# Performance work log

Hardware: AMD Instinct MI355X
Metric: run time of the kernel (lower is better)

Reference implementation:

```python
import jax, jax.numpy as jnp
import numpy as np

B, S, D, H = 2, 2048, 2048, 16
Dh = D // H


def _rotate_interleaved(t):
    # t: (..., Dh); pairs (x0,x1) -> (-x1, x0), interleaved
    t2 = t.reshape(t.shape[:-1] + (Dh // 2, 2))
    rot = jnp.stack([-t2[..., 1], t2[..., 0]], axis=-1)
    return rot.reshape(t.shape)


def _apply_rope(t, cos, sin):
    # t: (B,H,S,Dh); cos/sin: (S,Dh) broadcast over batch and heads
    return t * cos[None, None, :, :] + _rotate_interleaved(t) * sin[None, None, :, :]


def setup_inputs() -> dict:
    key = jax.random.key(0)
    ks = jax.random.split(key, 4)
    x = jax.random.normal(ks[0], (B, S, D), dtype=jnp.float32)
    wq = jax.random.normal(ks[1], (D, D), dtype=jnp.float32) * (D ** -0.5)
    wk = jax.random.normal(ks[2], (D, D), dtype=jnp.float32) * (D ** -0.5)
    wv = jax.random.normal(ks[3], (D, D), dtype=jnp.float32) * (D ** -0.5)
    # Real RoPE cos/sin tables: theta_i = 10000^{-2i/Dh}, interleaved layout
    inv_freq = 1.0 / (10000.0 ** (np.arange(0, Dh, 2, dtype=np.float32) / Dh))
    angles = np.arange(S, dtype=np.float32)[:, None] * inv_freq[None, :]  # (S, Dh/2)
    angles = np.repeat(angles, 2, axis=-1)  # (S, Dh) interleaved
    rope_cos = jnp.asarray(np.cos(angles))
    rope_sin = jnp.asarray(np.sin(angles))
    return {"x": x, "wq": wq, "wk": wk, "wv": wv,
            "rope_cos": rope_cos, "rope_sin": rope_sin}


def reference(x, wq, wk, wv, rope_cos, rope_sin):
    b, s, d = x.shape
    # QKV projections (torch Linear: y = x @ W^T), split into heads -> (B,H,S,Dh)
    def proj(w):
        return (x @ w.T).reshape(b, s, H, Dh).transpose(0, 2, 1, 3)
    q, k, v = proj(wq), proj(wk), proj(wv)
    cos, sin = rope_cos[:s], rope_sin[:s]
    q = _apply_rope(q, cos, sin)
    k = _apply_rope(k, cos, sin)
    # causal SDPA
    scores = jnp.einsum('bhqd,bhkd->bhqk', q, k) / jnp.sqrt(jnp.float32(Dh))
    causal = jnp.tril(jnp.ones((s, s), dtype=bool))
    scores = jnp.where(causal[None, None], scores, jnp.float32(-1e30))
    attn = jax.nn.softmax(scores, axis=-1)
    out = jnp.einsum('bhqk,bhkd->bhqd', attn, v)  # (B,H,S,Dh)
    # extra trailing softmax over head dim (as in source)
    out = jax.nn.softmax(out.astype(jnp.float32), axis=-1)
    return out.transpose(0, 2, 1, 3).reshape(b, s, -1)
```

## Files before the change

kernel.cpp:

```cpp
#include <hip/hip_runtime.h>

#define Bc 2
#define Sc 2048
#define Dc 2048
#define Hc 16
#define DHc 128

typedef _Float16 f16;
typedef __attribute__((ext_vector_type(4))) _Float16 v4h;
typedef __attribute__((ext_vector_type(8))) _Float16 v8h;
typedef __attribute__((ext_vector_type(4))) float v4f;
typedef __attribute__((ext_vector_type(16))) float v16f;
typedef __attribute__((ext_vector_type(4))) float f32x4;

__global__ void cvt_kernel(const float* __restrict__ x, const float* __restrict__ wq,
                           const float* __restrict__ wk, const float* __restrict__ wv,
                           f16* __restrict__ xh, f16* __restrict__ wqh,
                           f16* __restrict__ wkh, f16* __restrict__ wvh)
{
    int bid = blockIdx.x;
    const float* src; f16* dst; int idx;
    if (bid < 8192)       { src = x;  dst = xh;  idx = bid; }
    else if (bid < 12288) { src = wq; dst = wqh; idx = bid - 8192; }
    else if (bid < 16384) { src = wk; dst = wkh; idx = bid - 12288; }
    else                  { src = wv; dst = wvh; idx = bid - 16384; }
    int i = idx * 256 + threadIdx.x;
    f32x4 v = ((const f32x4*)src)[i];
    v4h hv; hv[0]=(f16)v[0]; hv[1]=(f16)v[1]; hv[2]=(f16)v[2]; hv[3]=(f16)v[3];
    ((v4h*)dst)[i] = hv;
}

__launch_bounds__(512, 2)
__global__ void proj256_kernel(const f16* __restrict__ xh, const f16* __restrict__ wall,
                               const float* __restrict__ cs, const float* __restrict__ sn,
                               f16* __restrict__ qh, f16* __restrict__ kh,
                               f16* __restrict__ vt)
{
    const int bid = blockIdx.x;
    const int swz = (bid & 7) * 96 + (bid >> 3);
    const int mt = swz & 31, nt = swz >> 5;
    const int m0 = mt * 128, n0 = nt * 256;

    const int tid = threadIdx.x;
    const int wid = tid >> 6, lane = tid & 63;
    const int wr = wid >> 2, wc = wid & 3;
    const int l15 = lane & 15, quad = lane >> 4;
    const int x7 = l15 & 7;

    __shared__ __align__(16) f16 lds[73728];

    const f16* aS[2]; const f16* bS[4];
    #pragma unroll
    for (int j = 0; j < 2; ++j) {
        int c = tid + j * 512;
        int r = c >> 3, s = c & 7;
        aS[j] = xh + (size_t)(m0 + r) * Dc + ((s ^ (r & 7)) * 8);
    }
    #pragma unroll
    for (int j = 0; j < 4; ++j) {
        int c = tid + j * 512;
        int r = c >> 3, s = c & 7;
        bS[j] = wall + (size_t)(n0 + r) * Dc + ((s ^ (r & 7)) * 8);
    }

#define STAGE(kt_, buf_) do {                                                   \
        const int _ko = (kt_) * 64;                                             \
        f16* _b = lds + (buf_) * 24576;                                         \
        _Pragma("unroll")                                                       \
        for (int j = 0; j < 2; ++j)                                             \
            __builtin_amdgcn_global_load_lds(                                   \
                (const __attribute__((address_space(1))) void*)(aS[j] + _ko),   \
                (__attribute__((address_space(3))) void*)(_b + j * 4096 + wid * 512), \
                16, 0, 0);                                                      \
        _Pragma("unroll")                                                       \
        for (int j = 0; j < 4; ++j)                                             \
            __builtin_amdgcn_global_load_lds(                                   \
                (const __attribute__((address_space(1))) void*)(bS[j] + _ko),   \
                (__attribute__((address_space(3))) void*)(_b + 8192 + j * 4096 + wid * 512), \
                16, 0, 0);                                                      \
    } while (0)

#define VMW12 asm volatile("s_waitcnt vmcnt(12)" ::: "memory")
#define VMW6  asm volatile("s_waitcnt vmcnt(6)"  ::: "memory")
#define VMW0  asm volatile("s_waitcnt vmcnt(0)"  ::: "memory")
#define LGKM0 asm volatile("s_waitcnt lgkmcnt(0)" ::: "memory")
#define BAR   __builtin_amdgcn_s_barrier()

    v4f acc[4][4];
    #pragma unroll
    for (int i = 0; i < 4; ++i)
        #pragma unroll
        for (int j = 0; j < 4; ++j)
            acc[i][j] = (v4f){0.f, 0.f, 0.f, 0.f};

    STAGE(0, 0);
    STAGE(1, 1);

    int bR = 0;
    int bSt = 2;

    #pragma unroll 1
    for (int t = 0; t < 32; ++t) {
        if (t + 2 < 32) { STAGE(t + 2, bSt); VMW12; }
        else if (t + 1 < 32) { VMW6; }
        else { VMW0; }
        BAR;

        {
            const f16* _Ab = lds + bR * 24576;
            const f16* _Bb = _Ab + 8192;
            v8h af[2][4], bf[2][4];
            #pragma unroll
            for (int kk = 0; kk < 2; ++kk) {
                #pragma unroll
                for (int mi = 0; mi < 4; ++mi)
                    af[kk][mi] = *(const v8h*)(_Ab + (wr * 64 + mi * 16 + l15) * 64
                                               + (((kk * 4 + quad) ^ x7) * 8));
                #pragma unroll
                for (int ni = 0; ni < 4; ++ni)
                    bf[kk][ni] = *(const v8h*)(_Bb + (wc * 64 + ni * 16 + l15) * 64
                                               + (((kk * 4 + quad) ^ x7) * 8));
            }
            __builtin_amdgcn_s_setprio(1);
            #pragma unroll
            for (int kk = 0; kk < 2; ++kk)
                #pragma unroll
                for (int mi = 0; mi < 4; ++mi)
                    #pragma unroll
                    for (int ni = 0; ni < 4; ++ni)
                        acc[mi][ni] = __builtin_amdgcn_mfma_f32_16x16x32_f16(
                            af[kk][mi], bf[kk][ni], acc[mi][ni], 0, 0, 0);
            __builtin_amdgcn_s_setprio(0);
        }

        LGKM0;
        BAR;

        bR  = (bR  == 2) ? 0 : bR  + 1;
        bSt = (bSt == 2) ? 0 : bSt + 1;
    }

#undef STAGE
#undef VMW12
#undef VMW6
#undef VMW0
#undef LGKM0
#undef BAR

    const int z = n0 >> 11;
    const int bb = m0 >> 11, s0 = m0 & 2047;

    if (z < 2) {
        f16 (*Ep)[264] = (f16(*)[264])lds;
        #pragma unroll
        for (int mi = 0; mi < 4; ++mi)
            #pragma unroll
            for (int ni = 0; ni < 4; ++ni)
                #pragma unroll
                for (int r = 0; r < 4; ++r)
                    Ep[wr * 64 + mi * 16 + quad * 4 + r][wc * 64 + ni * 16 + l15] =
                        (f16)acc[mi][ni][r];
        __syncthreads();
        f16* outp = (z == 0) ? qh : kh;
        const float scl = (z == 0) ? 0.08838834764831845f : 1.0f;
        #pragma unroll
        for (int it = 0; it < 8; ++it) {
            int ch = tid + it * 512, row = ch >> 5, c = ch & 31;
            v8h val = *(const v8h*)&Ep[row][c * 8];
            int s = s0 + row;
            int nn = (n0 & 2047) + c * 8;
            int h = nn >> 7, d0 = nn & 127;
            const float* cp = cs + (size_t)s * DHc + d0;
            const float* sp = sn + (size_t)s * DHc + d0;
            f32x4 ca = *(const f32x4*)cp, cb = *(const f32x4*)(cp + 4);
            f32x4 sa = *(const f32x4*)sp, sb = *(const f32x4*)(sp + 4);
            float v[8];
            #pragma unroll
            for (int j = 0; j < 8; ++j) v[j] = (float)val[j];
            v8h rv;
            rv[0] = (f16)((v[0]*ca[0] - v[1]*sa[0]) * scl);
            rv[1] = (f16)((v[1]*ca[1] + v[0]*sa[1]) * scl);
            rv[2] = (f16)((v[2]*ca[2] - v[3]*sa[2]) * scl);
            rv[3] = (f16)((v[3]*ca[3] + v[2]*sa[3]) * scl);
            rv[4] = (f16)((v[4]*cb[0] - v[5]*sb[0]) * scl);
            rv[5] = (f16)((v[5]*cb[1] + v[4]*sb[1]) * scl);
            rv[6] = (f16)((v[6]*cb[2] - v[7]*sb[2]) * scl);
            rv[7] = (f16)((v[7]*cb[3] + v[6]*sb[3]) * scl);
            *(v8h*)(outp + ((size_t)(bb * Hc + h) * Sc + s) * DHc + d0) = rv;
        }
    } else {
        f16 (*Ep)[136] = (f16(*)[136])lds;
        #pragma unroll
        for (int mi = 0; mi < 4; ++mi)
            #pragma unroll
            for (int ni = 0; ni < 4; ++ni)
                #pragma unroll
                for (int r = 0; r < 4; ++r)
                    Ep[wc * 64 + ni * 16 + l15][wr * 64 + mi * 16 + quad * 4 + r] =
                        (f16)acc[mi][ni][r];
        __syncthreads();
        #pragma unroll
        for (int it = 0; it < 8; ++it) {
            int ch = tid + it * 512, n = ch >> 4, cm = ch & 15;
            int nn = (n0 & 2047) + n;
            int h = nn >> 7, d = nn & 127;
            int s = s0 + cm * 8;
            *(v8h*)(vt + ((size_t)(bb * Hc + h) * DHc + d) * Sc + s) =
                *(const v8h*)&Ep[n][cm * 8];
        }
    }
}

__launch_bounds__(256)
__global__ void proj_kernel(const float* __restrict__ x, const float* __restrict__ wq,
                            const float* __restrict__ wk, const float* __restrict__ wv,
                            f16* __restrict__ qh, f16* __restrict__ kh, f16* __restrict__ vt)
{
    const int z = blockIdx.z;
    const float* w = (z == 0) ? wq : ((z == 1) ? wk : wv);
    const int m0 = blockIdx.x * 128, n0 = blockIdx.y * 128;
    const int tid = threadIdx.x, lane = tid & 63, wid = tid >> 6;
    const int wm = wid >> 1, wn = wid & 1;
    const int l15 = lane & 15, quad = lane >> 4;

    __shared__ __align__(16) f16 smem[2 * 128 * 72];
    f16 (*As)[72] = (f16(*)[72])smem;
    f16 (*Bs)[72] = (f16(*)[72])(smem + 128 * 72);

    v4f acc[4][4];
    for (int i = 0; i < 4; ++i)
        for (int j = 0; j < 4; ++j)
            acc[i][j] = (v4f){0.f, 0.f, 0.f, 0.f};

    for (int k0 = 0; k0 < Dc; k0 += 64) {
        __syncthreads();
        for (int it = 0; it < 4; ++it) {
            int chunk = tid + it * 256;
            int r = chunk >> 3, cc = chunk & 7;
            const f32x4* pa = (const f32x4*)(x + (size_t)(m0 + r) * Dc + k0 + cc * 8);
            f32x4 a0 = pa[0], a1 = pa[1];
            v8h ha;
            ha[0]=(f16)a0[0]; ha[1]=(f16)a0[1]; ha[2]=(f16)a0[2]; ha[3]=(f16)a0[3];
            ha[4]=(f16)a1[0]; ha[5]=(f16)a1[1]; ha[6]=(f16)a1[2]; ha[7]=(f16)a1[3];
            *(v8h*)&As[r][cc * 8] = ha;
            const f32x4* pb = (const f32x4*)(w + (size_t)(n0 + r) * Dc + k0 + cc * 8);
            f32x4 b0 = pb[0], b1 = pb[1];
            v8h hb;
            hb[0]=(f16)b0[0]; hb[1]=(f16)b0[1]; hb[2]=(f16)b0[2]; hb[3]=(f16)b0[3];
            hb[4]=(f16)b1[0]; hb[5]=(f16)b1[1]; hb[6]=(f16)b1[2]; hb[7]=(f16)b1[3];
            *(v8h*)&Bs[r][cc * 8] = hb;
        }
        __syncthreads();
        for (int kk = 0; kk < 2; ++kk) {
            v8h af[4], bf[4];
            for (int mi = 0; mi < 4; ++mi)
                af[mi] = *(const v8h*)&As[wm * 64 + mi * 16 + l15][kk * 32 + quad * 8];
            for (int ni = 0; ni < 4; ++ni)
                bf[ni] = *(const v8h*)&Bs[wn * 64 + ni * 16 + l15][kk * 32 + quad * 8];
            for (int mi = 0; mi < 4; ++mi)
                for (int ni = 0; ni < 4; ++ni)
                    acc[mi][ni] = __builtin_amdgcn_mfma_f32_16x16x32_f16(
                        af[mi], bf[ni], acc[mi][ni], 0, 0, 0);
        }
    }
    __syncthreads();
    f16 (*Ep)[136] = (f16(*)[136])smem;
    for (int mi = 0; mi < 4; ++mi)
        for (int ni = 0; ni < 4; ++ni)
            for (int r = 0; r < 4; ++r) {
                int ml = wm * 64 + mi * 16 + quad * 4 + r;
                int nl = wn * 64 + ni * 16 + l15;
                f16 val = (f16)acc[mi][ni][r];
                if (z == 2) Ep[nl][ml] = val;
                else        Ep[ml][nl] = val;
            }
    __syncthreads();
    const int b = m0 >> 11, s0 = m0 & 2047, h = n0 >> 7;
    if (z < 2) {
        f16* outp = (z == 0) ? qh : kh;
        for (int it = 0; it < 8; ++it) {
            int ch = tid + it * 256, row = ch >> 4, c = ch & 15;
            *(v8h*)(outp + ((size_t)((b * Hc + h) * Sc) + s0 + row) * DHc + c * 8) =
                *(const v8h*)&Ep[row][c * 8];
        }
    } else {
        for (int it = 0; it < 8; ++it) {
            int ch = tid + it * 256, row = ch >> 4, c = ch & 15;
            *(v8h*)(vt + ((size_t)((b * Hc + h) * DHc) + row) * Sc + s0 + c * 8) =
                *(const v8h*)&Ep[row][c * 8];
        }
    }
}

__global__ void rope_kernel(f16* __restrict__ qh, f16* __restrict__ kh,
                            const float* __restrict__ cs, const float* __restrict__ sn)
{
    int i  = blockIdx.x * 256 + threadIdx.x;
    int d2 = i & 63;
    int s  = (i >> 6) & (Sc - 1);
    int bh = i >> 17;
    f16* t = blockIdx.y ? kh : qh;
    float scale = blockIdx.y ? 1.0f : 0.08838834764831845f;
    float c  = cs[s * DHc + 2 * d2];
    float sv = sn[s * DHc + 2 * d2];
    f16* p = t + ((size_t)bh * Sc + s) * DHc + 2 * d2;
    float t0 = (float)p[0], t1 = (float)p[1];
    p[0] = (f16)((t0 * c - t1 * sv) * scale);
    p[1] = (f16)((t1 * c + t0 * sv) * scale);
}

__launch_bounds__(256, 2)
__global__ void attn_kernel(const f16* __restrict__ qh, const f16* __restrict__ kh,
                            const f16* __restrict__ vt, float* __restrict__ out)
{
    const int L = blockIdx.x;
    const int slot = L >> 3;
    const int bh = (L & 7) * 4 + (slot >> 3);
    const int p  = slot & 7;
    const int b = bh >> 4, h = bh & 15;
    const int tid = threadIdx.x, lane = tid & 63, w = tid >> 6;
    const int l31 = lane & 31, half = lane >> 5;
    const int sw = l31 & 7;

    __shared__ __align__(16) f16 smem[32768];
    f16* ksm = smem;
    f16* vsm = smem + 16384;

    const size_t bhoff = (size_t)bh * Sc * DHc;

    const f16* ksrc[4]; const f16* vsrc[4];
    f16* kdst[4]; f16* vdst[4];
    #pragma unroll
    for (int j = 0; j < 4; ++j) {
        int slot0 = j * 256 + w * 64;
        {   int r = (slot0 >> 4) + (lane >> 4);
            int c = (lane & 15) ^ (r & 7);
            ksrc[j] = kh + bhoff + (size_t)r * DHc + c * 8;
            kdst[j] = ksm + slot0 * 8; }
        {   int r = (slot0 >> 3) + (lane >> 3);
            int c = (lane & 7) ^ (r & 7);
            vsrc[j] = vt + bhoff + (size_t)r * Sc + c * 8;
            vdst[j] = vsm + slot0 * 8; }
    }

#define STAGE(kt_, buf_) do {                                                   \
        int _ko = (kt_) * 64 * DHc;                                             \
        int _vo = (kt_) * 64;                                                   \
        int _lb = (buf_) * 8192;                                                \
        _Pragma("unroll")                                                       \
        for (int j = 0; j < 4; ++j) {                                           \
            __builtin_amdgcn_global_load_lds(                                   \
                (const __attribute__((address_space(1))) void*)(ksrc[j] + _ko), \
                (__attribute__((address_space(3))) void*)(kdst[j] + _lb), 16, 0, 0); \
            __builtin_amdgcn_global_load_lds(                                   \
                (const __attribute__((address_space(1))) void*)(vsrc[j] + _vo), \
                (__attribute__((address_space(3))) void*)(vdst[j] + _lb), 16, 0, 0); \
        } } while (0)

    const int qtA = 15 - p;
    const int nktA = 2 * qtA + 2;

    int ibuf = 0;
    STAGE(0, 0);

    #pragma unroll 1
    for (int ph = 0; ph < 2; ++ph) {
        const int qt  = ph ? p : qtA;
        const int nkt = 2 * qt + 2;
        const int q0  = qt * 128 + w * 32;
        const int qg  = q0 + l31;

        v8h qf[8];
        const f16* qrow = qh + bhoff + (size_t)qg * DHc;
        #pragma unroll
        for (int s = 0; s < 8; ++s)
            qf[s] = *(const v8h*)(qrow + s * 16 + half * 8);

        float l_run = 0.f;
        v16f o[4];
        #pragma unroll
        for (int i = 0; i < 4; ++i)
            #pragma unroll
            for (int r = 0; r < 16; ++r) o[i][r] = 0.f;

        #pragma unroll 1
        for (int kt = 0; kt < nkt; ++kt, ++ibuf) {
            __syncthreads();
            const int buf = ibuf & 1;
            const int ni = ibuf + 1;
            if (ni < 34) {
                int tn = (ni < nktA) ? ni : ni - nktA;
                STAGE(tn, ni & 1);
            }
            if (q0 + 31 < kt * 64) continue;

            const f16* kbuf = ksm + buf * 8192;
            const f16* vbuf = vsm + buf * 8192;
            const bool do1 = (kt * 64 + 32 <= q0 + 31);

            v16f st0, st1;
            #pragma unroll
            for (int r = 0; r < 16; ++r) { st0[r] = 0.f; st1[r] = 0.f; }
            #pragma unroll
            for (int s = 0; s < 8; ++s) {
                int c = ((s * 2 + half) ^ sw) * 8;
                v8h kf0 = *(const v8h*)(kbuf + l31 * 128 + c);
                st0 = __builtin_amdgcn_mfma_f32_32x32x16_f16(kf0, qf[s], st0, 0, 0, 0);
                if (do1) {
                    v8h kf1 = *(const v8h*)(kbuf + (32 + l31) * 128 + c);
                    st1 = __builtin_amdgcn_mfma_f32_32x32x16_f16(kf1, qf[s], st1, 0, 0, 0);
                }
            }

            float sum = 0.f;
            #pragma unroll
            for (int r = 0; r < 16; ++r) {
                int key = kt * 64 + (r & 3) + 8 * (r >> 2) + 4 * half;
                float sv = (key > qg) ? -1e30f : st0[r];
                float pe = __expf(sv);
                st0[r] = pe; sum += pe;
            }
            if (do1) {
                #pragma unroll
                for (int r = 0; r < 16; ++r) {
                    int key = kt * 64 + 32 + (r & 3) + 8 * (r >> 2) + 4 * half;
                    float sv = (key > qg) ? -1e30f : st1[r];
                    float pe = __expf(sv);
                    st1[r] = pe; sum += pe;
                }
            }
            sum += __shfl_xor(sum, 32);
            l_run += sum;

            #pragma unroll
            for (int s2 = 0; s2 < 4; ++s2) {
                v4h bfr;
                bfr[0]=(f16)st0[4*s2]; bfr[1]=(f16)st0[4*s2+1];
                bfr[2]=(f16)st0[4*s2+2]; bfr[3]=(f16)st0[4*s2+3];
                int c = ((s2 ^ sw) * 8) + half * 4;
                #pragma unroll
                for (int dt = 0; dt < 4; ++dt) {
                    v4h vf = *(const v4h*)(vbuf + (dt * 32 + l31) * 64 + c);
                    o[dt] = __builtin_amdgcn_mfma_f32_32x32x8f16(vf, bfr, o[dt], 0, 0, 0);
                }
            }
            if (do1) {
                #pragma unroll
                for (int s2 = 0; s2 < 4; ++s2) {
                    v4h bfr;
                    bfr[0]=(f16)st1[4*s2]; bfr[1]=(f16)st1[4*s2+1];
                    bfr[2]=(f16)st1[4*s2+2]; bfr[3]=(f16)st1[4*s2+3];
                    int c = (((4 + s2) ^ sw) * 8) + half * 4;
                    #pragma unroll
                    for (int dt = 0; dt < 4; ++dt) {
                        v4h vf = *(const v4h*)(vbuf + (dt * 32 + l31) * 64 + c);
                        o[dt] = __builtin_amdgcn_mfma_f32_32x32x8f16(vf, bfr, o[dt], 0, 0, 0);
                    }
                }
            }
        }

        float inv = 1.f / l_run;
        float mxd = -1e30f;
        #pragma unroll
        for (int dt = 0; dt < 4; ++dt)
            #pragma unroll
            for (int r = 0; r < 16; ++r) {
                o[dt][r] *= inv;
                mxd = fmaxf(mxd, o[dt][r]);
            }
        mxd = fmaxf(mxd, __shfl_xor(mxd, 32));
        float sd = 0.f;
        #pragma unroll
        for (int dt = 0; dt < 4; ++dt)
            #pragma unroll
            for (int r = 0; r < 16; ++r) {
                float t = __expf(o[dt][r] - mxd);
                o[dt][r] = t;
                sd += t;
            }
        sd += __shfl_xor(sd, 32);
        float rinv = 1.f / sd;

        float* orow = out + (size_t)(b * Sc + qg) * Dc + h * DHc;
        #pragma unroll
        for (int dt = 0; dt < 4; ++dt)
            #pragma unroll
            for (int g = 0; g < 4; ++g) {
                f32x4 vv;
                vv[0] = o[dt][4*g+0] * rinv;
                vv[1] = o[dt][4*g+1] * rinv;
                vv[2] = o[dt][4*g+2] * rinv;
                vv[3] = o[dt][4*g+3] * rinv;
                *(f32x4*)(orow + dt * 32 + g * 8 + half * 4) = vv;
            }
    }
#undef STAGE
}

extern "C" void kernel_launch(void* const* d_in, const int* in_sizes, int n_in,
                              void* d_out, int out_size, void* d_ws, size_t ws_size,
                              hipStream_t stream)
{
    const float* x  = (const float*)d_in[0];
    const float* wq = (const float*)d_in[1];
    const float* wk = (const float*)d_in[2];
    const float* wv = (const float*)d_in[3];
    const float* cs = (const float*)d_in[4];
    const float* sn = (const float*)d_in[5];
    float* out = (float*)d_out;

    const size_t tsz = (size_t)Bc * Hc * Sc * DHc;
    f16* qh = (f16*)d_ws;
    f16* kh = qh + tsz;
    f16* vt = kh + tsz;

    if (ws_size >= 11 * tsz) {
        f16* xh  = vt + tsz;
        f16* wqh = xh + tsz;
        f16* wkh = wqh + tsz / 2;
        f16* wvh = wkh + tsz / 2;
        cvt_kernel<<<20480, 256, 0, stream>>>(x, wq, wk, wv, xh, wqh, wkh, wvh);
        proj256_kernel<<<768, 512, 0, stream>>>(xh, wqh, cs, sn, qh, kh, vt);
    } else {
        proj_kernel<<<dim3(32, 16, 3), 256, 0, stream>>>(x, wq, wk, wv, qh, kh, vt);
        rope_kernel<<<dim3(16384, 2), 256, 0, stream>>>(qh, kh, cs, sn);
    }
    attn_kernel<<<256, 256, 0, stream>>>(qh, kh, vt, out);
}
```

Before: 322.3 us.

## Split GEMM k-tile into two phases interleaving loads; one q-tile per attention block

Result: no change. 320.6 us (-0.5%).

```diff
diff --git a/kernel.cpp b/kernel.cpp
--- a/kernel.cpp
+++ b/kernel.cpp
@@ -63,29 +63,55 @@
         bS[j] = wall + (size_t)(n0 + r) * Dc + ((s ^ (r & 7)) * 8);
     }
 
-#define STAGE(kt_, buf_) do {                                                   \
+#define GLD(src_, dst_)                                                         \
+    __builtin_amdgcn_global_load_lds(                                           \
+        (const __attribute__((address_space(1))) void*)(src_),                  \
+        (__attribute__((address_space(3))) void*)(dst_), 16, 0, 0)
+
+#define STAGE_P0(kt_, buf_) do {                                                \
         const int _ko = (kt_) * 64;                                             \
         f16* _b = lds + (buf_) * 24576;                                         \
-        _Pragma("unroll")                                                       \
-        for (int j = 0; j < 2; ++j)                                             \
-            __builtin_amdgcn_global_load_lds(                                   \
-                (const __attribute__((address_space(1))) void*)(aS[j] + _ko),   \
-                (__attribute__((address_space(3))) void*)(_b + j * 4096 + wid * 512), \
-                16, 0, 0);                                                      \
-        _Pragma("unroll")                                                       \
-        for (int j = 0; j < 4; ++j)                                             \
-            __builtin_amdgcn_global_load_lds(                                   \
-                (const __attribute__((address_space(1))) void*)(bS[j] + _ko),   \
-                (__attribute__((address_space(3))) void*)(_b + 8192 + j * 4096 + wid * 512), \
-                16, 0, 0);                                                      \
+        GLD(aS[0] + _ko, _b + wid * 512);                                       \
+        GLD(aS[1] + _ko, _b + 4096 + wid * 512);                                \
+        GLD(bS[0] + _ko, _b + 8192 + wid * 512);                                \
     } while (0)
 
-#define VMW12 asm volatile("s_waitcnt vmcnt(12)" ::: "memory")
+#define STAGE_P1(kt_, buf_) do {                                                \
+        const int _ko = (kt_) * 64;                                             \
+        f16* _b = lds + (buf_) * 24576;                                         \
+        GLD(bS[1] + _ko, _b + 8192 + 4096  + wid * 512);                        \
+        GLD(bS[2] + _ko, _b + 8192 + 8192  + wid * 512);                        \
+        GLD(bS[3] + _ko, _b + 8192 + 12288 + wid * 512);                        \
+    } while (0)
+
 #define VMW6  asm volatile("s_waitcnt vmcnt(6)"  ::: "memory")
 #define VMW0  asm volatile("s_waitcnt vmcnt(0)"  ::: "memory")
 #define LGKM0 asm volatile("s_waitcnt lgkmcnt(0)" ::: "memory")
 #define BAR   __builtin_amdgcn_s_barrier()
 
+#define PHASE(kk_, bR_) do {                                                    \
+        const f16* _Ab = lds + (bR_) * 24576;                                   \
+        const f16* _Bb = _Ab + 8192;                                            \
+        v8h af[4], bf[4];                                                       \
+        _Pragma("unroll")                                                       \
+        for (int mi = 0; mi < 4; ++mi)                                          \
+            af[mi] = *(const v8h*)(_Ab + (wr * 64 + mi * 16 + l15) * 64         \
+                                   + ((((kk_) * 4 + quad) ^ x7) * 8));          \
+        _Pragma("unroll")                                                       \
+        for (int ni = 0; ni < 4; ++ni)                                          \
+            bf[ni] = *(const v8h*)(_Bb + (wc * 64 + ni * 16 + l15) * 64         \
+                                   + ((((kk_) * 4 + quad) ^ x7) * 8));          \
+        PH_TAIL;                                                                \
+        __builtin_amdgcn_s_setprio(1);                                          \
+        _Pragma("unroll")                                                       \
+        for (int mi = 0; mi < 4; ++mi)                                          \
+            _Pragma("unroll")                                                   \
+            for (int ni = 0; ni < 4; ++ni)                                      \
+                acc[mi][ni] = __builtin_amdgcn_mfma_f32_16x16x32_f16(           \
+                    af[mi], bf[ni], acc[mi][ni], 0, 0, 0);                      \
+        __builtin_amdgcn_s_setprio(0);                                          \
+    } while (0)
+
     v4f acc[4][4];
     #pragma unroll
     for (int i = 0; i < 4; ++i)
@@ -93,46 +119,29 @@
         for (int j = 0; j < 4; ++j)
             acc[i][j] = (v4f){0.f, 0.f, 0.f, 0.f};
 
-    STAGE(0, 0);
-    STAGE(1, 1);
+    STAGE_P0(0, 0); STAGE_P1(0, 0);
+    STAGE_P0(1, 1); STAGE_P1(1, 1);
+    VMW6;
+    BAR;
 
     int bR = 0;
     int bSt = 2;
 
     #pragma unroll 1
     for (int t = 0; t < 32; ++t) {
-        if (t + 2 < 32) { STAGE(t + 2, bSt); VMW12; }
-        else if (t + 1 < 32) { VMW6; }
-        else { VMW0; }
+        {
+#define PH_TAIL do { if (t + 2 < 32) STAGE_P0(t + 2, bSt); BAR; } while (0)
+            PHASE(0, bR);
+#undef PH_TAIL
+        }
         BAR;
-
         {
-            const f16* _Ab = lds + bR * 24576;
-            const f16* _Bb = _Ab + 8192;
-            v8h af[2][4], bf[2][4];
-            #pragma unroll
-            for (int kk = 0; kk < 2; ++kk) {
-                #pragma unroll
-                for (int mi = 0; mi < 4; ++mi)
-                    af[kk][mi] = *(const v8h*)(_Ab + (wr * 64 + mi * 16 + l15) * 64
-                                               + (((kk * 4 + quad) ^ x7) * 8));
-                #pragma unroll
-                for (int ni = 0; ni < 4; ++ni)
-                    bf[kk][ni] = *(const v8h*)(_Bb + (wc * 64 + ni * 16 + l15) * 64
-                                               + (((kk * 4 + quad) ^ x7) * 8));
-            }
-            __builtin_amdgcn_s_setprio(1);
-            #pragma unroll
-            for (int kk = 0; kk < 2; ++kk)
-                #pragma unroll
-                for (int mi = 0; mi < 4; ++mi)
-                    #pragma unroll
-                    for (int ni = 0; ni < 4; ++ni)
-                        acc[mi][ni] = __builtin_amdgcn_mfma_f32_16x16x32_f16(
-                            af[kk][mi], bf[kk][ni], acc[mi][ni], 0, 0, 0);
-            __builtin_amdgcn_s_setprio(0);
-        }
-
+#define PH_TAIL do { if (t + 2 < 32) STAGE_P1(t + 2, bSt);                      \
+                     if (t < 30) { VMW6; } else { VMW0; }                       \
+                     BAR; } while (0)
+            PHASE(1, bR);
+#undef PH_TAIL
+        }
         LGKM0;
         BAR;
 
@@ -140,12 +149,14 @@
         bSt = (bSt == 2) ? 0 : bSt + 1;
     }
 
-#undef STAGE
-#undef VMW12
+#undef STAGE_P0
+#undef STAGE_P1
+#undef GLD
 #undef VMW6
 #undef VMW0
 #undef LGKM0
 #undef BAR
+#undef PHASE
 
     const int z = n0 >> 11;
     const int bb = m0 >> 11, s0 = m0 & 2047;
@@ -314,9 +325,9 @@
                             const f16* __restrict__ vt, float* __restrict__ out)
 {
     const int L = blockIdx.x;
-    const int slot = L >> 3;
-    const int bh = (L & 7) * 4 + (slot >> 3);
-    const int p  = slot & 7;
+    const int s_ = L >> 3;
+    const int bh = (L & 7) * 4 + (s_ >> 4);
+    const int qt = 15 - (s_ & 15);
     const int b = bh >> 4, h = bh & 15;
     const int tid = threadIdx.x, lane = tid & 63, w = tid >> 6;
     const int l31 = lane & 31, half = lane >> 5;
@@ -357,144 +368,131 @@
                 (__attribute__((address_space(3))) void*)(vdst[j] + _lb), 16, 0, 0); \
         } } while (0)
 
-    const int qtA = 15 - p;
-    const int nktA = 2 * qtA + 2;
-
-    int ibuf = 0;
+    const int nkt = 2 * qt + 2;
+    const int q0  = qt * 128 + w * 32;
+    const int qg  = q0 + l31;
+
+    v8h qf[8];
+    const f16* qrow = qh + bhoff + (size_t)qg * DHc;
+    #pragma unroll
+    for (int s = 0; s < 8; ++s)
+        qf[s] = *(const v8h*)(qrow + s * 16 + half * 8);
+
+    float l_run = 0.f;
+    v16f o[4];
+    #pragma unroll
+    for (int i = 0; i < 4; ++i)
+        #pragma unroll
+        for (int r = 0; r < 16; ++r) o[i][r] = 0.f;
+
     STAGE(0, 0);
 
     #pragma unroll 1
-    for (int ph = 0; ph < 2; ++ph) {
-        const int qt  = ph ? p : qtA;
-        const int nkt = 2 * qt + 2;
-        const int q0  = qt * 128 + w * 32;
-        const int qg  = q0 + l31;
-
-        v8h qf[8];
-        const f16* qrow = qh + bhoff + (size_t)qg * DHc;
-        #pragma unroll
-        for (int s = 0; s < 8; ++s)
-            qf[s] = *(const v8h*)(qrow + s * 16 + half * 8);
-
-        float l_run = 0.f;
-        v16f o[4];
-        #pragma unroll
-        for (int i = 0; i < 4; ++i)
-            #pragma unroll
-            for (int r = 0; r < 16; ++r) o[i][r] = 0.f;
-
-        #pragma unroll 1
-        for (int kt = 0; kt < nkt; ++kt, ++ibuf) {
-            __syncthreads();
-            const int buf = ibuf & 1;
-            const int ni = ibuf + 1;
-            if (ni < 34) {
-                int tn = (ni < nktA) ? ni : ni - nktA;
-                STAGE(tn, ni & 1);
+    for (int kt = 0; kt < nkt; ++kt) {
+        __syncthreads();
+        if (kt + 1 < nkt) STAGE(kt + 1, (kt + 1) & 1);
+        if (q0 + 31 < kt * 64) continue;
+
+        const f16* kbuf = ksm + (kt & 1) * 8192;
+        const f16* vbuf = vsm + (kt & 1) * 8192;
+        const bool do1 = (kt * 64 + 32 <= q0 + 31);
+
+        v16f st0, st1;
+        #pragma unroll
+        for (int r = 0; r < 16; ++r) { st0[r] = 0.f; st1[r] = 0.f; }
+        #pragma unroll
+        for (int s = 0; s < 8; ++s) {
+            int c = ((s * 2 + half) ^ sw) * 8;
+            v8h kf0 = *(const v8h*)(kbuf + l31 * 128 + c);
+            st0 = __builtin_amdgcn_mfma_f32_32x32x16_f16(kf0, qf[s], st0, 0, 0, 0);
+            if (do1) {
+                v8h kf1 = *(const v8h*)(kbuf + (32 + l31) * 128 + c);
+                st1 = __builtin_amdgcn_mfma_f32_32x32x16_f16(kf1, qf[s], st1, 0, 0, 0);
             }
-            if (q0 + 31 < kt * 64) continue;
-
-            const f16* kbuf = ksm + buf * 8192;
-            const f16* vbuf = vsm + buf * 8192;
-            const bool do1 = (kt * 64 + 32 <= q0 + 31);
-
-            v16f st0, st1;
-            #pragma unroll
-            for (int r = 0; r < 16; ++r) { st0[r] = 0.f; st1[r] = 0.f; }
-            #pragma unroll
-            for (int s = 0; s < 8; ++s) {
-                int c = ((s * 2 + half) ^ sw) * 8;
-                v8h kf0 = *(const v8h*)(kbuf + l31 * 128 + c);
-                st0 = __builtin_amdgcn_mfma_f32_32x32x16_f16(kf0, qf[s], st0, 0, 0, 0);
-                if (do1) {
-                    v8h kf1 = *(const v8h*)(kbuf + (32 + l31) * 128 + c);
-                    st1 = __builtin_amdgcn_mfma_f32_32x32x16_f16(kf1, qf[s], st1, 0, 0, 0);
-                }
-            }
-
-            float sum = 0.f;
+        }
+
+        float sum = 0.f;
+        #pragma unroll
+        for (int r = 0; r < 16; ++r) {
+            int key = kt * 64 + (r & 3) + 8 * (r >> 2) + 4 * half;
+            float sv = (key > qg) ? -1e30f : st0[r];
+            float pe = __expf(sv);
+            st0[r] = pe; sum += pe;
+        }
+        if (do1) {
             #pragma unroll
             for (int r = 0; r < 16; ++r) {
-                int key = kt * 64 + (r & 3) + 8 * (r >> 2) + 4 * half;
-                float sv = (key > qg) ? -1e30f : st0[r];
+                int key = kt * 64 + 32 + (r & 3) + 8 * (r >> 2) + 4 * half;
+                float sv = (key > qg) ? -1e30f : st1[r];
                 float pe = __expf(sv);
-                st0[r] = pe; sum += pe;
+                st1[r] = pe; sum += pe;
             }
-            if (do1) {
-                #pragma unroll
-                for (int r = 0; r < 16; ++r) {
-                    int key = kt * 64 + 32 + (r & 3) + 8 * (r >> 2) + 4 * half;
-                    float sv = (key > qg) ? -1e30f : st1[r];
-                    float pe = __expf(sv);
-                    st1[r] = pe; sum += pe;
-                }
+        }
+        sum += __shfl_xor(sum, 32);
+        l_run += sum;
+
+        #pragma unroll
+        for (int s2 = 0; s2 < 4; ++s2) {
+            v4h bfr;
+            bfr[0]=(f16)st0[4*s2]; bfr[1]=(f16)st0[4*s2+1];
+            bfr[2]=(f16)st0[4*s2+2]; bfr[3]=(f16)st0[4*s2+3];
+            int c = ((s2 ^ sw) * 8) + half * 4;
+            #pragma unroll
+            for (int dt = 0; dt < 4; ++dt) {
+                v4h vf = *(const v4h*)(vbuf + (dt * 32 + l31) * 64 + c);
+                o[dt] = __builtin_amdgcn_mfma_f32_32x32x8f16(vf, bfr, o[dt], 0, 0, 0);
             }
-            sum += __shfl_xor(sum, 32);
-            l_run += sum;
-
+        }
+        if (do1) {
             #pragma unroll
             for (int s2 = 0; s2 < 4; ++s2) {
                 v4h bfr;
-                bfr[0]=(f16)st0[4*s2]; bfr[1]=(f16)st0[4*s2+1];
-                bfr[2]=(f16)st0[4*s2+2]; bfr[3]=(f16)st0[4*s2+3];
-                int c = ((s2 ^ sw) * 8) + half * 4;
+                bfr[0]=(f16)st1[4*s2]; bfr[1]=(f16)st1[4*s2+1];
+                bfr[2]=(f16)st1[4*s2+2]; bfr[3]=(f16)st1[4*s2+3];
+                int c = (((4 + s2) ^ sw) * 8) + half * 4;
                 #pragma unroll
                 for (int dt = 0; dt < 4; ++dt) {
                     v4h vf = *(const v4h*)(vbuf + (dt * 32 + l31) * 64 + c);
                     o[dt] = __builtin_amdgcn_mfma_f32_32x32x8f16(vf, bfr, o[dt], 0, 0, 0);
                 }
             }
-            if (do1) {
-                #pragma unroll
-                for (int s2 = 0; s2 < 4; ++s2) {
-                    v4h bfr;
-                    bfr[0]=(f16)st1[4*s2]; bfr[1]=(f16)st1[4*s2+1];
-                    bfr[2]=(f16)st1[4*s2+2]; bfr[3]=(f16)st1[4*s2+3];
-                    int c = (((4 + s2) ^ sw) * 8) + half * 4;
-                    #pragma unroll
-                    for (int dt = 0; dt < 4; ++dt) {
-                        v4h vf = *(const v4h*)(vbuf + (dt * 32 + l31) * 64 + c);
-                        o[dt] = __builtin_amdgcn_mfma_f32_32x32x8f16(vf, bfr, o[dt], 0, 0, 0);
-                    }
-                }
-            }
-        }
-
-        float inv = 1.f / l_run;
-        float mxd = -1e30f;
-        #pragma unroll
-        for (int dt = 0; dt < 4; ++dt)
-            #pragma unroll
-            for (int r = 0; r < 16; ++r) {
-                o[dt][r] *= inv;
-                mxd = fmaxf(mxd, o[dt][r]);
-            }
-        mxd = fmaxf(mxd, __shfl_xor(mxd, 32));
-        float sd = 0.f;
-        #pragma unroll
-        for (int dt = 0; dt < 4; ++dt)
-            #pragma unroll
-            for (int r = 0; r < 16; ++r) {
-                float t = __expf(o[dt][r] - mxd);
-                o[dt][r] = t;
-                sd += t;
-            }
-        sd += __shfl_xor(sd, 32);
-        float rinv = 1.f / sd;
-
-        float* orow = out + (size_t)(b * Sc + qg) * Dc + h * DHc;
-        #pragma unroll
-        for (int dt = 0; dt < 4; ++dt)
-            #pragma unroll
-            for (int g = 0; g < 4; ++g) {
-                f32x4 vv;
-                vv[0] = o[dt][4*g+0] * rinv;
-                vv[1] = o[dt][4*g+1] * rinv;
-                vv[2] = o[dt][4*g+2] * rinv;
-                vv[3] = o[dt][4*g+3] * rinv;
-                *(f32x4*)(orow + dt * 32 + g * 8 + half * 4) = vv;
-            }
-    }
+        }
+    }
+
+    float inv = 1.f / l_run;
+    float mxd = -1e30f;
+    #pragma unroll
+    for (int dt = 0; dt < 4; ++dt)
+        #pragma unroll
+        for (int r = 0; r < 16; ++r) {
+            o[dt][r] *= inv;
+            mxd = fmaxf(mxd, o[dt][r]);
+        }
+    mxd = fmaxf(mxd, __shfl_xor(mxd, 32));
+    float sd = 0.f;
+    #pragma unroll
+    for (int dt = 0; dt < 4; ++dt)
+        #pragma unroll
+        for (int r = 0; r < 16; ++r) {
+            float t = __expf(o[dt][r] - mxd);
+            o[dt][r] = t;
+            sd += t;
+        }
+    sd += __shfl_xor(sd, 32);
+    float rinv = 1.f / sd;
+
+    float* orow = out + (size_t)(b * Sc + qg) * Dc + h * DHc;
+    #pragma unroll
+    for (int dt = 0; dt < 4; ++dt)
+        #pragma unroll
+        for (int g = 0; g < 4; ++g) {
+            f32x4 vv;
+            vv[0] = o[dt][4*g+0] * rinv;
+            vv[1] = o[dt][4*g+1] * rinv;
+            vv[2] = o[dt][4*g+2] * rinv;
+            vv[3] = o[dt][4*g+3] * rinv;
+            *(f32x4*)(orow + dt * 32 + g * 8 + half * 4) = vv;
+        }
 #undef STAGE
 }
 
@@ -526,5 +524,5 @@
         proj_kernel<<<dim3(32, 16, 3), 256, 0, stream>>>(x, wq, wk, wv, qh, kh, vt);
         rope_kernel<<<dim3(16384, 2), 256, 0, stream>>>(qh, kh, cs, sn);
     }
-    attn_kernel<<<256, 256, 0, stream>>>(qh, kh, vt, out);
+    attn_kernel<<<512, 256, 0, stream>>>(qh, kh, vt, out);
 }
```
